# Performance work log

Measured on AMD Instinct MI355X. Metric: run time of the kernel, lower is better.

## Reference

```python
import jax, jax.numpy as jnp
import numpy as np

WS = 10      # window_size
HID = 32     # hidden_dim
B, T = 1024, 4096


def setup_inputs() -> dict:
    key = jax.random.key(0)
    k = jax.random.split(key, 7)
    returns = jax.random.normal(k[0], (B, T), dtype=jnp.float32) * 0.01
    W1 = jax.random.normal(k[1], (WS, HID), dtype=jnp.float32) * (1.0 / np.sqrt(WS))
    b1 = jnp.zeros((HID,), dtype=jnp.float32)
    W2 = jax.random.normal(k[2], (HID, HID), dtype=jnp.float32) * (1.0 / np.sqrt(HID))
    b2 = jnp.zeros((HID,), dtype=jnp.float32)
    W3 = jax.random.normal(k[3], (HID, 1), dtype=jnp.float32) * (1.0 / np.sqrt(HID))
    b3 = jnp.zeros((1,), dtype=jnp.float32)
    return {"returns": returns, "W1": W1, "b1": b1, "W2": W2, "b2": b2, "W3": W3, "b3": b3}


def reference(returns, W1, b1, W2, b2, W3, b3):
    ws = W1.shape[0]
    Bb, Tt = returns.shape
    # Unfold all sliding windows at once: windows[b, i, :] = returns[b, i:i+ws]
    # (window ending just before timestep t = i + ws)
    idx = jnp.arange(Tt - ws)[:, None] + jnp.arange(ws)[None, :]  # [T-ws, ws]
    windows = returns[:, idx]                                     # [B, T-ws, ws]
    h = jax.nn.relu(windows @ W1 + b1)                            # [B, T-ws, HID]
    h = jax.nn.relu(h @ W2 + b2)                                  # [B, T-ws, HID]
    out = 0.5 * jax.nn.sigmoid((h @ W3 + b3).squeeze(-1))         # [B, T-ws]
    # H_local[:, t] = out[:, t-ws] for t >= ws; first ws columns copy column ws
    head = jnp.broadcast_to(out[:, :1], (Bb, ws))                 # [B, ws]
    return jnp.concatenate([head, out], axis=1)                   # [B, T]
```

## Files before the change

kernel.cpp:

```cpp
#include <hip/hip_runtime.h>
#include <math.h>

typedef _Float16 f16x8  __attribute__((ext_vector_type(8)));
typedef _Float16 h2v    __attribute__((ext_vector_type(2)));
typedef float    f32x16 __attribute__((ext_vector_type(16)));
typedef float    f32x4  __attribute__((ext_vector_type(4)));
typedef __fp16   h2a    __attribute__((ext_vector_type(2)));
typedef unsigned u32x4  __attribute__((ext_vector_type(4)));

#define WS    10
#define HID   32
#define BDIM  256
#define NWAVE 4
#define GN    32
#define TILE  1024
#define NGRP  (TILE / GN)

__device__ inline unsigned pack2u(float a, float b) {
    h2a t = __builtin_amdgcn_cvt_pkrtz(a, b);
    return __builtin_bit_cast(unsigned, t);
}
__device__ inline unsigned relu2(unsigned u) {
    h2v x = __builtin_bit_cast(h2v, u);
    h2v z = {(_Float16)0.0f, (_Float16)0.0f};
    return __builtin_bit_cast(unsigned, __builtin_elementwise_max(x, z));
}

__global__ __launch_bounds__(BDIM, 4)
void hurst_mlp_v3(const float* __restrict__ returns,
                  const float* __restrict__ W1, const float* __restrict__ b1,
                  const float* __restrict__ W2, const float* __restrict__ b2,
                  const float* __restrict__ W3, const float* __restrict__ b3,
                  float* __restrict__ out, int T)
{
    __shared__ __align__(16) _Float16 Xh[TILE][16];

    const int tid  = threadIdx.x;
    const int wid  = tid >> 6;
    const int lane = tid & 63;
    const int n    = lane & 31;
    const int hi   = lane >> 5;
    const int permidx = (lane ^ 32) << 2;

    f32x16 b1v, b2v, w3v;
    #pragma unroll
    for (int i = 0; i < 4; ++i) {
        const f32x4 v1 = ((const f32x4*)b1)[2 * i + hi];
        const f32x4 v2 = ((const f32x4*)b2)[2 * i + hi];
        const f32x4 v3 = ((const f32x4*)W3)[2 * i + hi];
        #pragma unroll
        for (int o = 0; o < 4; ++o) {
            b1v[4 * i + o] = v1[o];
            b2v[4 * i + o] = v2[o];
            w3v[4 * i + o] = v3[o];
        }
    }
    const float b3s = b3[0];

    f16x8 a1, a2lo, a2hi;
    #pragma unroll
    for (int jj = 0; jj < 8; ++jj) {
        const int k  = 8 * hi + jj;
        a1[jj] = (k < WS) ? (_Float16)W1[k * HID + n] : (_Float16)0.0f;
        const int kf = (k & 3) | ((k & 4) << 1) | ((k & 8) >> 1);
        a2lo[jj] = (_Float16)W2[kf * HID + n];
        a2hi[jj] = (_Float16)W2[(16 + kf) * HID + n];
    }

    const int    b   = blockIdx.y;
    const int    t0  = blockIdx.x * TILE;
    const size_t row = (size_t)b * (size_t)T;

    if (blockIdx.x != 0) {
        const int base = t0 + 4 * tid - 12;
        f32x4 fl0 = *(const f32x4*)&returns[row + base];
        f32x4 fl1 = *(const f32x4*)&returns[row + base + 4];
        f32x4 fl2 = *(const f32x4*)&returns[row + base + 8];
        f32x4 fl3 = *(const f32x4*)&returns[row + base + 12];
        float fl[16];
        #pragma unroll
        for (int o = 0; o < 4; ++o) {
            fl[o] = fl0[o]; fl[4 + o] = fl1[o]; fl[8 + o] = fl2[o]; fl[12 + o] = fl3[o];
        }
        #pragma unroll
        for (int j = 0; j < 4; ++j) {
            const int m = 4 * tid + j;
            u32x4 lo, hi4;
            lo[0]  = pack2u(fl[j + 2],  fl[j + 3]);
            lo[1]  = pack2u(fl[j + 4],  fl[j + 5]);
            lo[2]  = pack2u(fl[j + 6],  fl[j + 7]);
            lo[3]  = pack2u(fl[j + 8],  fl[j + 9]);
            hi4[0] = pack2u(fl[j + 10], fl[j + 11]);
            hi4[1] = 0u; hi4[2] = 0u; hi4[3] = 0u;
            *(u32x4*)&Xh[m][0] = lo;
            *(u32x4*)&Xh[m][8] = hi4;
        }
    } else {
        #pragma unroll
        for (int j = 0; j < 4; ++j) {
            const int m  = 4 * tid + j;
            const int ws = (m >= WS) ? (m - WS) : 0;
            float fw[WS];
            #pragma unroll
            for (int k = 0; k < WS; ++k) fw[k] = returns[row + ws + k];
            u32x4 lo, hi4;
            lo[0]  = pack2u(fw[0], fw[1]);
            lo[1]  = pack2u(fw[2], fw[3]);
            lo[2]  = pack2u(fw[4], fw[5]);
            lo[3]  = pack2u(fw[6], fw[7]);
            hi4[0] = pack2u(fw[8], fw[9]);
            hi4[1] = 0u; hi4[2] = 0u; hi4[3] = 0u;
            *(u32x4*)&Xh[m][0] = lo;
            *(u32x4*)&Xh[m][8] = hi4;
        }
    }
    __syncthreads();

    f16x8 xb = *(const f16x8*)&Xh[wid * GN + n][hi * 8];
    for (int g = wid; g < NGRP; g += NWAVE) {
        const int gn = (g + NWAVE < NGRP) ? (g + NWAVE) : g;
        const f16x8 xb_next = *(const f16x8*)&Xh[gn * GN + n][hi * 8];

        f32x16 d1 = __builtin_amdgcn_mfma_f32_32x32x16_f16(a1, xb, b1v, 0, 0, 0);

        u32x4 blo_u, bhi_u;
        #pragma unroll
        for (int i = 0; i < 4; ++i) {
            blo_u[i] = relu2(pack2u(d1[2 * i],     d1[2 * i + 1]));
            bhi_u[i] = relu2(pack2u(d1[8 + 2 * i], d1[9 + 2 * i]));
        }

        f32x16 d2 = __builtin_amdgcn_mfma_f32_32x32x16_f16(
                        a2lo, __builtin_bit_cast(f16x8, blo_u), b2v, 0, 0, 0);
        d2 = __builtin_amdgcn_mfma_f32_32x32x16_f16(
                        a2hi, __builtin_bit_cast(f16x8, bhi_u), d2, 0, 0, 0);

        float acc = 0.0f;
        #pragma unroll
        for (int r = 0; r < 16; ++r)
            acc = fmaf(fmaxf(d2[r], 0.0f), w3v[r], acc);
        acc += __builtin_bit_cast(float,
                 __builtin_amdgcn_ds_bpermute(permidx, __builtin_bit_cast(int, acc)));

        const float o = 0.5f * __builtin_amdgcn_rcpf(1.0f + __expf(-(acc + b3s)));
        if (hi == 0)
            out[row + (size_t)(t0 + g * GN + n)] = o;

        xb = xb_next;
    }
}

extern "C" void kernel_launch(void* const* d_in, const int* in_sizes, int n_in,
                              void* d_out, int out_size, void* d_ws, size_t ws_size,
                              hipStream_t stream) {
    const float* returns = (const float*)d_in[0];
    const float* W1      = (const float*)d_in[1];
    const float* b1      = (const float*)d_in[2];
    const float* W2      = (const float*)d_in[3];
    const float* b2      = (const float*)d_in[4];
    const float* W3      = (const float*)d_in[5];
    const float* b3      = (const float*)d_in[6];
    float* out = (float*)d_out;

    const int T = 4096;
    const int B = out_size / T;

    dim3 grid(T / TILE, B, 1);
    dim3 block(BDIM, 1, 1);
    hurst_mlp_v3<<<grid, block, 0, stream>>>(returns, W1, b1, W2, b2, W3, b3, out, T);
}
```

Before: 106.4 us.

## Process one full row per block and load windows directly from global memory

The LDS staging of fp16 windows and the block-wide barrier are removed. Each lane now reads its window straight from global memory (unaligned 32-byte and 8-byte loads) and packs it to fp16 in registers. The grid changes from 4 tiles per row to one block per row, so each block loops over all 128 groups and the block count drops fourfold. This avoids LDS traffic and per-tile prologue work, but it relies on cache for the overlapping window reads, loses the software prefetch of the next group, and leaves fewer, longer blocks to hide latency.

```diff
diff --git a/kernel.cpp b/kernel.cpp
--- a/kernel.cpp
+++ b/kernel.cpp
@@ -13,8 +13,8 @@
 #define BDIM  256
 #define NWAVE 4
 #define GN    32
-#define TILE  1024
-#define NGRP  (TILE / GN)
+#define T_LEN 4096
+#define NGRP  (T_LEN / GN)
 
 __device__ inline unsigned pack2u(float a, float b) {
     h2a t = __builtin_amdgcn_cvt_pkrtz(a, b);
@@ -27,14 +27,12 @@
 }
 
 __global__ __launch_bounds__(BDIM, 4)
-void hurst_mlp_v3(const float* __restrict__ returns,
-                  const float* __restrict__ W1, const float* __restrict__ b1,
-                  const float* __restrict__ W2, const float* __restrict__ b2,
-                  const float* __restrict__ W3, const float* __restrict__ b3,
-                  float* __restrict__ out, int T)
+void hurst_row(const float* __restrict__ returns,
+               const float* __restrict__ W1, const float* __restrict__ b1,
+               const float* __restrict__ W2, const float* __restrict__ b2,
+               const float* __restrict__ W3, const float* __restrict__ b3,
+               float* __restrict__ out)
 {
-    __shared__ __align__(16) _Float16 Xh[TILE][16];
-
     const int tid  = threadIdx.x;
     const int wid  = tid >> 6;
     const int lane = tid & 63;
@@ -67,59 +65,28 @@
         a2hi[jj] = (_Float16)W2[(16 + kf) * HID + n];
     }
 
-    const int    b   = blockIdx.y;
-    const int    t0  = blockIdx.x * TILE;
-    const size_t row = (size_t)b * (size_t)T;
+    const float* rptr = returns + (size_t)blockIdx.x * T_LEN;
+    float*       optr = out     + (size_t)blockIdx.x * T_LEN;
 
-    if (blockIdx.x != 0) {
-        const int base = t0 + 4 * tid - 12;
-        f32x4 fl0 = *(const f32x4*)&returns[row + base];
-        f32x4 fl1 = *(const f32x4*)&returns[row + base + 4];
-        f32x4 fl2 = *(const f32x4*)&returns[row + base + 8];
-        f32x4 fl3 = *(const f32x4*)&returns[row + base + 12];
-        float fl[16];
-        #pragma unroll
-        for (int o = 0; o < 4; ++o) {
-            fl[o] = fl0[o]; fl[4 + o] = fl1[o]; fl[8 + o] = fl2[o]; fl[12 + o] = fl3[o];
+    for (int g = wid; g < NGRP; g += NWAVE) {
+        const int t  = g * GN + n;
+        const int ws = (t >= WS) ? (t - WS) : 0;
+
+        u32x4 xu;
+        if (hi == 0) {
+            float w8[8];
+            __builtin_memcpy(w8, &rptr[ws], 32);
+            xu[0] = pack2u(w8[0], w8[1]);
+            xu[1] = pack2u(w8[2], w8[3]);
+            xu[2] = pack2u(w8[4], w8[5]);
+            xu[3] = pack2u(w8[6], w8[7]);
+        } else {
+            float w2[2];
+            __builtin_memcpy(w2, &rptr[ws + 8], 8);
+            xu[0] = pack2u(w2[0], w2[1]);
+            xu[1] = 0u; xu[2] = 0u; xu[3] = 0u;
         }
-        #pragma unroll
-        for (int j = 0; j < 4; ++j) {
-            const int m = 4 * tid + j;
-            u32x4 lo, hi4;
-            lo[0]  = pack2u(fl[j + 2],  fl[j + 3]);
-            lo[1]  = pack2u(fl[j + 4],  fl[j + 5]);
-            lo[2]  = pack2u(fl[j + 6],  fl[j + 7]);
-            lo[3]  = pack2u(fl[j + 8],  fl[j + 9]);
-            hi4[0] = pack2u(fl[j + 10], fl[j + 11]);
-            hi4[1] = 0u; hi4[2] = 0u; hi4[3] = 0u;
-            *(u32x4*)&Xh[m][0] = lo;
-            *(u32x4*)&Xh[m][8] = hi4;
-        }
-    } else {
-        #pragma unroll
-        for (int j = 0; j < 4; ++j) {
-            const int m  = 4 * tid + j;
-            const int ws = (m >= WS) ? (m - WS) : 0;
-            float fw[WS];
-            #pragma unroll
-            for (int k = 0; k < WS; ++k) fw[k] = returns[row + ws + k];
-            u32x4 lo, hi4;
-            lo[0]  = pack2u(fw[0], fw[1]);
-            lo[1]  = pack2u(fw[2], fw[3]);
-            lo[2]  = pack2u(fw[4], fw[5]);
-            lo[3]  = pack2u(fw[6], fw[7]);
-            hi4[0] = pack2u(fw[8], fw[9]);
-            hi4[1] = 0u; hi4[2] = 0u; hi4[3] = 0u;
-            *(u32x4*)&Xh[m][0] = lo;
-            *(u32x4*)&Xh[m][8] = hi4;
-        }
-    }
-    __syncthreads();
-
-    f16x8 xb = *(const f16x8*)&Xh[wid * GN + n][hi * 8];
-    for (int g = wid; g < NGRP; g += NWAVE) {
-        const int gn = (g + NWAVE < NGRP) ? (g + NWAVE) : g;
-        const f16x8 xb_next = *(const f16x8*)&Xh[gn * GN + n][hi * 8];
+        const f16x8 xb = __builtin_bit_cast(f16x8, xu);
 
         f32x16 d1 = __builtin_amdgcn_mfma_f32_32x32x16_f16(a1, xb, b1v, 0, 0, 0);
 
@@ -144,9 +111,7 @@
 
         const float o = 0.5f * __builtin_amdgcn_rcpf(1.0f + __expf(-(acc + b3s)));
         if (hi == 0)
-            out[row + (size_t)(t0 + g * GN + n)] = o;
-
-        xb = xb_next;
+            optr[t] = o;
     }
 }
 
@@ -162,10 +127,9 @@
     const float* b3      = (const float*)d_in[6];
     float* out = (float*)d_out;
 
-    const int T = 4096;
-    const int B = out_size / T;
+    const int B = out_size / T_LEN;
 
-    dim3 grid(T / TILE, B, 1);
+    dim3 grid(B, 1, 1);
     dim3 block(BDIM, 1, 1);
-    hurst_mlp_v3<<<grid, block, 0, stream>>>(returns, W1, b1, W2, b2, W3, b3, out, T);
+    hurst_row<<<grid, block, 0, stream>>>(returns, W1, b1, W2, b2, W3, b3, out);
 }
```

Result: no change. 106.7 us (+0.3%).
